# Kernel tuning notes

Measured on AMD Instinct MI355X. Metric: run time of the kernel, lower is better.

## Reference

```python
import jax, jax.numpy as jnp
import numpy as np

B, T, DIM = 4, 1024, 2048
N_HEADS, N_KV_HEADS = 32, 8
HEAD_DIM = DIM // N_HEADS  # 64
N_REPS = N_HEADS // N_KV_HEADS  # 4


def setup_inputs() -> dict:
    key = jax.random.key(0)
    ks = jax.random.split(key, 8)
    # RoPE tables: theta = 10000^{-2i/d}, positions 0..T-1
    inv_freq = 1.0 / (10000.0 ** (jnp.arange(0, HEAD_DIM, 2, dtype=jnp.float32) / HEAD_DIM))
    angles = jnp.arange(T, dtype=jnp.float32)[:, None] * inv_freq[None, :]  # (T, HEAD_DIM//2)
    s = 0.02
    return {
        "input": jax.random.normal(ks[0], (B, T, DIM), jnp.float32),
        "freqs_cos": jnp.cos(angles),
        "freqs_sin": jnp.sin(angles),
        "mask": jnp.tril(jnp.ones((T, T), dtype=bool)),  # causal boolean mask
        "wq": s * jax.random.normal(ks[1], (DIM, DIM), jnp.float32),
        "wk": s * jax.random.normal(ks[2], (N_KV_HEADS * HEAD_DIM, DIM), jnp.float32),
        "wv": s * jax.random.normal(ks[3], (N_KV_HEADS * HEAD_DIM, DIM), jnp.float32),
        "wo": s * jax.random.normal(ks[4], (DIM, DIM), jnp.float32),
        "curr_pos": 0,
    }


def _apply_rope(x, cos, sin):
    # x: (B, T, H, D); cos/sin: (T, D//2). Complex multiply on (even, odd) pairs.
    xr = x[..., 0::2]
    xi = x[..., 1::2]
    c = cos[None, :, None, :]
    s = sin[None, :, None, :]
    out_r = xr * c - xi * s
    out_i = xr * s + xi * c
    return jnp.stack([out_r, out_i], axis=-1).reshape(x.shape)


def reference(input, freqs_cos, freqs_sin, mask, wq, wk, wv, wo, curr_pos):
    Bv, Tv = input.shape[0], input.shape[1]
    qs = (input @ wq.T).reshape(Bv, Tv, N_HEADS, HEAD_DIM)
    ks = (input @ wk.T).reshape(Bv, Tv, N_KV_HEADS, HEAD_DIM)
    vs = (input @ wv.T).reshape(Bv, Tv, N_KV_HEADS, HEAD_DIM)
    qs = _apply_rope(qs, freqs_cos, freqs_sin)
    ks = _apply_rope(ks, freqs_cos, freqs_sin)

    # KV cache (prefill path: curr_pos == 0, fresh cache of length 2T)
    kv_cache = jnp.zeros((Bv, 2 * Tv, N_KV_HEADS, HEAD_DIM, 2), input.dtype)
    kv_cache = kv_cache.at[:, curr_pos:curr_pos + Tv, :, :, 0].set(ks)
    kv_cache = kv_cache.at[:, curr_pos:curr_pos + Tv, :, :, 1].set(vs)
    k_all = kv_cache[:, :curr_pos + Tv, :, :, 0]
    v_all = kv_cache[:, :curr_pos + Tv, :, :, 1]

    # GQA: broadcast each kv head across its query-head group (avoid repeat_interleave copy)
    S = k_all.shape[1]
    q = qs.transpose(0, 2, 1, 3).reshape(Bv, N_KV_HEADS, N_REPS, Tv, HEAD_DIM)
    k = k_all.transpose(0, 2, 1, 3)  # (B, KVH, S, D)
    v = v_all.transpose(0, 2, 1, 3)

    scale = 1.0 / jnp.sqrt(jnp.asarray(HEAD_DIM, input.dtype))
    scores = jnp.einsum("bgrqd,bgkd->bgrqk", q, k) * scale  # (B, KVH, REPS, T, S)
    neg = jnp.asarray(jnp.finfo(input.dtype).min, input.dtype)
    scores = jnp.where(mask[None, None, None, :, :S], scores, neg)
    attn = jax.nn.softmax(scores, axis=-1)
    out = jnp.einsum("bgrqk,bgkd->bgrqd", attn, v)
    out = out.reshape(Bv, N_HEADS, Tv, HEAD_DIM).transpose(0, 2, 1, 3).reshape(Bv, Tv, DIM)
    return out @ wo.T
```

## Files before the change

kernel.cpp:

```cpp
#include <hip/hip_runtime.h>
#include <cstdint>

typedef __bf16 bf16x8 __attribute__((ext_vector_type(8)));
typedef float  f32x4  __attribute__((ext_vector_type(4)));
typedef float  f32x16 __attribute__((ext_vector_type(16)));
typedef float  float8v __attribute__((ext_vector_type(8)));
typedef unsigned short ushort8v __attribute__((ext_vector_type(8)));
typedef unsigned short ushort4v __attribute__((ext_vector_type(4)));
typedef unsigned int   uint4v   __attribute__((ext_vector_type(4)));

__device__ __forceinline__ unsigned short f2b(float f) {
  uint32_t u = __builtin_bit_cast(uint32_t, f);
  u += 0x7FFFu + ((u >> 16) & 1u);
  return (unsigned short)(u >> 16);
}
__device__ __forceinline__ float b2f(unsigned short h) {
  uint32_t u = ((uint32_t)h) << 16;
  return __builtin_bit_cast(float, u);
}
__device__ __forceinline__ unsigned int cvtpk(float lo, float hi_) {
  unsigned int r;
  asm("v_cvt_pk_bf16_f32 %0, %1, %2" : "=v"(r) : "v"(lo), "v"(hi_));
  return r;
}

__device__ __forceinline__ void async16(const void* g, void* l) {
  __builtin_amdgcn_global_load_lds(
      (const __attribute__((address_space(1))) void*)g,
      (__attribute__((address_space(3))) void*)l, 16, 0, 0);
}

#define WAITVM(N)  __builtin_amdgcn_s_waitcnt(0x0F70 | ((N) & 15))
#define WAITLGKM0  __builtin_amdgcn_s_waitcnt(0xC07F)

struct CvtArgs {
  const float* src[5];
  unsigned short* dst[5];
  long n[5];
};
__global__ void cvt5_kernel(CvtArgs a) {
  long base = (long)blockIdx.x * blockDim.x + threadIdx.x;
  long gstride = (long)gridDim.x * blockDim.x;
#pragma unroll 1
  for (int sg = 0; sg < 5; ++sg) {
    const float* s = a.src[sg];
    unsigned short* d = a.dst[sg];
    long n8 = a.n[sg] >> 3;
    for (long i = base; i < n8; i += gstride) {
      float8v f = *(const float8v*)(s + i * 8);
      ushort8v o;
#pragma unroll
      for (int j = 0; j < 8; ++j) o[j] = f2b(f[j]);
      *(ushort8v*)(d + i * 8) = o;
    }
  }
}

template<bool F32OUT, int BN, int GX>
__global__ __launch_bounds__(512, 1)
void gemm8p(const unsigned short* __restrict__ Ag, const unsigned short* __restrict__ Wg,
            void* __restrict__ Cp, int M, int N) {
  constexpr int K = 2048;
  constexpr int NF = BN / 64;
  constexpr int BL = BN / 128;
  constexpr int VN = 4 + 2 * BL;
  constexpr int VT1 = (BN == 256) ? 6 : 4;
  constexpr int VT2 = (BN == 256) ? 4 : 3;
  constexpr int VT3 = (BN == 256) ? 2 : 1;
  constexpr int ASLOT = 16384;
  constexpr int BSLOT = BN * 64;
  constexpr int CPX = 2 * GX;

  extern __shared__ char lds_c[];

  const int tid = threadIdx.x;
  const int wave = tid >> 6, lane = tid & 63;
  const int wm = wave >> 2, wn = wave & 3;
  const int lr = lane & 15, lg = lane >> 4;

  const int flat = blockIdx.y * GX + blockIdx.x;
  const int swz = (flat & 7) * CPX + (flat >> 3);
  const int m0 = (swz / GX) * 256, n0 = (swz % GX) * BN;

  const int laneSw = (lr >> 1) * 128 + (((((lr & 1) << 2) | lg) ^ (lr >> 1)) << 4);
  const int aoff = wm * 8192 + laneSw;
  const int boff = wn * NF * 1024 + laneSw;

  f32x4 acc[8][NF] = {};

  auto stageHT = [&](int s) {
    const int ty = s & 3;
    const int kh = (s >> 1) & 1;
    const int buf = (s >> 2) & 1;
    const int kc = (s >> 2) * 64 + kh * 32;
    if (ty == 0 || ty == 2) {
      char* slot = lds_c + (buf * 2 + kh) * ASLOT;
#pragma unroll
      for (int j = 0; j < 2; ++j) {
        int q = (tid + 512 * j) * 16;
        int R = q >> 7, g2L = ((q >> 4) & 7) ^ (R & 7);
        int row = R * 2 + (g2L >> 2), kg = g2L & 3;
        async16(Ag + (size_t)(m0 + row) * K + kc + kg * 8, slot + q);
      }
    } else {
      char* slot = lds_c + 65536 + (buf * 2 + kh) * BSLOT;
#pragma unroll
      for (int j = 0; j < BL; ++j) {
        int q = (tid + 512 * j) * 16;
        int R = q >> 7, g2L = ((q >> 4) & 7) ^ (R & 7);
        int row = R * 2 + (g2L >> 2), kg = g2L & 3;
        async16(Wg + (size_t)(n0 + row) * K + kc + kg * 8, slot + q);
      }
    }
  };

#define PHASE(BUF, KH, MH, VM, ...)                                           \
  {                                                                           \
    const char* As_ = lds_c + ((BUF) * 2 + (KH)) * ASLOT;                     \
    const char* Bs_ = lds_c + 65536 + ((BUF) * 2 + (KH)) * BSLOT;             \
    bf16x8 af_[4], bf_[NF];                                                   \
    _Pragma("unroll") for (int mi = 0; mi < 4; ++mi)                          \
      af_[mi] = *(const bf16x8*)(As_ + aoff + (MH) * 4096 + mi * 1024);       \
    _Pragma("unroll") for (int ni = 0; ni < NF; ++ni)                         \
      bf_[ni] = *(const bf16x8*)(Bs_ + boff + ni * 1024);                     \
    __VA_ARGS__;                                                              \
    WAITVM(VM);                                                               \
    __builtin_amdgcn_s_barrier();                                             \
    WAITLGKM0;                                                                \
    __builtin_amdgcn_sched_barrier(0);                                        \
    __builtin_amdgcn_s_setprio(1);                                            \
    _Pragma("unroll") for (int mi = 0; mi < 4; ++mi)                          \
      _Pragma("unroll") for (int ni = 0; ni < NF; ++ni)                       \
        acc[(MH) * 4 + mi][ni] = __builtin_amdgcn_mfma_f32_16x16x32_bf16(     \
            af_[mi], bf_[ni], acc[(MH) * 4 + mi][ni], 0, 0, 0);               \
    __builtin_amdgcn_s_setprio(0);                                            \
    __builtin_amdgcn_s_barrier();                                             \
  }

#pragma unroll
  for (int s = 0; s < 6; ++s) stageHT(s);
  WAITVM(VN);
  __builtin_amdgcn_s_barrier();

#pragma unroll 2
  for (int kt = 0; kt < 30; ++kt) {
    const int buf = kt & 1;
    const int s0 = kt * 4 + 6;
    PHASE(buf, 0, 0, VN, stageHT(s0));
    PHASE(buf, 0, 1, VN, stageHT(s0 + 1));
    PHASE(buf, 1, 0, VN, stageHT(s0 + 2));
    PHASE(buf, 1, 1, VN, stageHT(s0 + 3));
  }
  PHASE(0, 0, 0, VN, stageHT(126));
  PHASE(0, 0, 1, VN, stageHT(127));
  PHASE(0, 1, 0, VT1, (void)0);
  PHASE(0, 1, 1, VT2, (void)0);
  PHASE(1, 0, 0, VT3, (void)0);
  PHASE(1, 0, 1, 0, (void)0);
  PHASE(1, 1, 0, 0, (void)0);
  PHASE(1, 1, 1, 0, (void)0);
#undef PHASE

#pragma unroll
  for (int mig = 0; mig < 8; ++mig) {
#pragma unroll
    for (int j = 0; j < 4; ++j) {
      int row = m0 + wm * 128 + mig * 16 + lg * 4 + j;
#pragma unroll
      for (int ni = 0; ni < NF; ++ni) {
        int col = n0 + wn * (NF * 16) + ni * 16 + lr;
        float v = acc[mig][ni][j];
        if (F32OUT) ((float*)Cp)[(size_t)row * N + col] = v;
        else        ((unsigned short*)Cp)[(size_t)row * N + col] = f2b(v);
      }
    }
  }
}

__global__ __launch_bounds__(256)
void ropekv_kernel(unsigned short* __restrict__ qkv,
                   const float* __restrict__ cosb, const float* __restrict__ sinb,
                   unsigned short* __restrict__ vt) {
  const int tt0 = blockIdx.x * 64;
  const int kvh = blockIdx.y;
  const int b   = blockIdx.z;
  const int tid = threadIdx.x;

  {
    int r = tid >> 2, c0 = (tid & 3) * 16;
    int t = tt0 + r;
    unsigned short* kp = qkv + (size_t)(b * 1024 + t) * 3072 + 2048 + kvh * 64 + c0;
    const float* cb = cosb + t * 32 + c0 / 2;
    const float* sb = sinb + t * 32 + c0 / 2;
    ushort8v x0 = *(const ushort8v*)kp;
    ushort8v x1 = *(const ushort8v*)(kp + 8);
    float8v c = *(const float8v*)cb;
    float8v s = *(const float8v*)sb;
    ushort8v o0, o1;
#pragma unroll
    for (int j = 0; j < 4; ++j) {
      float xr = b2f(x0[2 * j]), xi = b2f(x0[2 * j + 1]);
      o0[2 * j]     = f2b(xr * c[j] - xi * s[j]);
      o0[2 * j + 1] = f2b(xr * s[j] + xi * c[j]);
    }
#pragma unroll
    for (int j = 0; j < 4; ++j) {
      float xr = b2f(x1[2 * j]), xi = b2f(x1[2 * j + 1]);
      o1[2 * j]     = f2b(xr * c[4 + j] - xi * s[4 + j]);
      o1[2 * j + 1] = f2b(xr * s[4 + j] + xi * c[4 + j]);
    }
    *(ushort8v*)kp = o0;
    *(ushort8v*)(kp + 8) = o1;
  }

  __shared__ unsigned short lT[64 * 68];
#pragma unroll
  for (int i = 0; i < 2; ++i) {
    int r = i * 32 + (tid >> 3), c = (tid & 7) * 8;
    const unsigned short* src = qkv + (size_t)(b * 1024 + tt0 + r) * 3072 + 2560 + kvh * 64 + c;
    ushort8v v = *(const ushort8v*)src;
    ushort4v a, b4;
#pragma unroll
    for (int j = 0; j < 4; ++j) { a[j] = v[j]; b4[j] = v[j + 4]; }
    *(ushort4v*)&lT[r * 68 + c]     = a;
    *(ushort4v*)&lT[r * 68 + c + 4] = b4;
  }
  __syncthreads();
#pragma unroll
  for (int i = 0; i < 2; ++i) {
    int d = tid & 63;
    int tt = i * 4 + (tid >> 6);
    ushort8v o;
#pragma unroll
    for (int j = 0; j < 8; ++j) o[j] = lT[(tt * 8 + j) * 68 + d];
    *(ushort8v*)&vt[((size_t)((b * 8 + kvh) * 64 + d)) * 1024 + tt0 + tt * 8] = o;
  }
}

__global__ __launch_bounds__(256, 2)
void attn_kernel(const unsigned short* __restrict__ qkv, const unsigned short* __restrict__ vt,
                 const float* __restrict__ cosb, const float* __restrict__ sinb,
                 unsigned short* __restrict__ ob) {
  const int flat = (blockIdx.z * 8 + blockIdx.y) * 16 + blockIdx.x;
  const int swzb = (flat & 7) * 64 + (flat >> 3);
  const int bx = swzb & 15, kvh = (swzb >> 4) & 7, b = swzb >> 7;

  const int tid = threadIdx.x, wave = tid >> 6, lane = tid & 63;
  const int l31 = lane & 31, hi = lane >> 5;
  const int h = kvh * 4 + wave;

  const int qth = 31 - bx, qtl = bx;
  const int q0h = qth * 32, q0l = qtl * 32;
  const int nth = qth / 4 + 1, ntl = qtl / 4 + 1;
  const int ntot = nth + ntl;

  __shared__ unsigned short lK[2][128 * 64];
  __shared__ unsigned short lVt[2][64 * 128];

  auto ldq = [&](int q0, bf16x8* qf) {
    int t = q0 + l31;
    const unsigned short* qp = qkv + (size_t)(b * 1024 + t) * 3072 + h * 64;
#pragma unroll
    for (int dk = 0; dk < 4; ++dk) {
      ushort8v q = *(const ushort8v*)(qp + dk * 16 + hi * 8);
      f32x4 c4 = *(const f32x4*)(cosb + t * 32 + dk * 8 + hi * 4);
      f32x4 s4 = *(const f32x4*)(sinb + t * 32 + dk * 8 + hi * 4);
      ushort8v o;
#pragma unroll
      for (int j = 0; j < 4; ++j) {
        float xr = b2f(q[2 * j]), xi = b2f(q[2 * j + 1]);
        o[2 * j]     = f2b(xr * c4[j] - xi * s4[j]);
        o[2 * j + 1] = f2b(xr * s4[j] + xi * c4[j]);
      }
      qf[dk] = __builtin_bit_cast(bf16x8, o);
    }
  };

  const unsigned short* kg = qkv + (size_t)(b * 1024) * 3072 + 2048 + kvh * 64;
  const unsigned short* vg = vt + (size_t)(b * 8 + kvh) * 64 * 1024;

  auto stage = [&](int kvb, int bi) {
    const int sr  = tid >> 3;
    const int scb = (tid & 7) * 16;
#pragma unroll
    for (int i = 0; i < 4; ++i) {
      int r = i * 32 + sr;
      int cb = scb ^ ((r & 7) << 4);
      async16(kg + (size_t)(kvb + r) * 3072 + (cb >> 1), &lK[bi][r * 64 + (scb >> 1)]);
    }
    const int rv0 = tid >> 4;
    const int scv = (tid & 15) * 16;
#pragma unroll
    for (int i = 0; i < 4; ++i) {
      int rv = i * 16 + rv0;
      int cbv = scv ^ ((rv & 15) << 4);
      async16(vg + (size_t)rv * 1024 + kvb + (cbv >> 1), &lVt[bi][rv * 128 + (scv >> 1)]);
    }
  };

  bf16x8 qf[4];
  f32x16 oacc[2] = {};
  float m2 = -3e38f, l_run = 0.f;
  int q0 = q0h;

  ldq(q0h, qf);

  const float SC = 0.125f * 1.44269504f;

  auto chunk64 = [&](int cur, int ckvb, int c, bool lastT) {
    f32x16 sd[2] = {};
    __builtin_amdgcn_s_setprio(1);
#pragma unroll
    for (int s = 0; s < 2; ++s) {
      const int krow = c * 64 + s * 32 + l31;
      const char* kr = (const char*)lK[cur] + krow * 128;
      const int swz = (krow & 7) << 4;
#pragma unroll
      for (int dk = 0; dk < 4; ++dk) {
        bf16x8 kf = *(const bf16x8*)(kr + ((dk * 32 + hi * 16) ^ swz));
        sd[s] = __builtin_amdgcn_mfma_f32_32x32x16_bf16(kf, qf[dk], sd[s], 0, 0, 0);
      }
    }
    __builtin_amdgcn_s_setprio(0);

#pragma unroll
    for (int s = 0; s < 2; ++s)
#pragma unroll
      for (int r = 0; r < 16; ++r) {
        float v = sd[s][r] * SC;
        if (lastT) {
          int kvg = ckvb + s * 32 + (r & 3) + 8 * (r >> 2) + 4 * hi;
          if (kvg > q0 + l31) v = -3e38f;
        }
        sd[s][r] = v;
      }
    float pm = sd[0][0];
#pragma unroll
    for (int s = 0; s < 2; ++s)
#pragma unroll
      for (int r = 0; r < 16; ++r) pm = fmaxf(pm, sd[s][r]);
    pm = fmaxf(pm, __shfl_xor(pm, 32));
    if (!__all(pm <= m2 + 11.0f)) {
      float mnew = fmaxf(m2, pm);
      float alpha = exp2f(m2 - mnew);
      m2 = mnew;
      l_run *= alpha;
#pragma unroll
      for (int db = 0; db < 2; ++db)
#pragma unroll
        for (int r = 0; r < 16; ++r) oacc[db][r] *= alpha;
    }
    float tsum = 0.f;
#pragma unroll
    for (int s = 0; s < 2; ++s)
#pragma unroll
      for (int r = 0; r < 16; ++r) { float p = exp2f(sd[s][r] - m2); sd[s][r] = p; tsum += p; }
    tsum += __shfl_xor(tsum, 32);
    l_run += tsum;

    bf16x8 pf[2][2];
#pragma unroll
    for (int s = 0; s < 2; ++s)
#pragma unroll
      for (int kc = 0; kc < 2; ++kc) {
        unsigned int cA = cvtpk(sd[s][8 * kc + 0], sd[s][8 * kc + 1]);
        unsigned int cB = cvtpk(sd[s][8 * kc + 4], sd[s][8 * kc + 5]);
        unsigned int cC = cvtpk(sd[s][8 * kc + 2], sd[s][8 * kc + 3]);
        unsigned int cD = cvtpk(sd[s][8 * kc + 6], sd[s][8 * kc + 7]);
        unsigned int xA = __shfl_xor(cA, 32), xB = __shfl_xor(cB, 32);
        unsigned int xC = __shfl_xor(cC, 32), xD = __shfl_xor(cD, 32);
        uint4v u;
        u[0] = hi ? xB : cA;
        u[1] = hi ? xD : cC;
        u[2] = hi ? cB : xA;
        u[3] = hi ? cD : xC;
        pf[s][kc] = __builtin_bit_cast(bf16x8, u);
      }

    __builtin_amdgcn_s_setprio(1);
#pragma unroll
    for (int db = 0; db < 2; ++db) {
      const int row = db * 32 + l31;
      const char* vr = (const char*)lVt[cur] + row * 256;
      const int vswz = (row & 15) << 4;
#pragma unroll
      for (int s = 0; s < 2; ++s)
#pragma unroll
        for (int kc = 0; kc < 2; ++kc) {
          bf16x8 vf = *(const bf16x8*)(vr + ((c * 128 + s * 64 + kc * 32 + hi * 16) ^ vswz));
          oacc[db] = __builtin_amdgcn_mfma_f32_32x32x16_bf16(vf, pf[s][kc], oacc[db], 0, 0, 0);
        }
    }
    __builtin_amdgcn_s_setprio(0);
  };

  auto writeOut = [&](int q0w) {
    float inv = 1.0f / l_run;
    unsigned short* orow = ob + (size_t)(b * 1024 + q0w + l31) * 2048 + h * 64;
#pragma unroll
    for (int db = 0; db < 2; ++db)
#pragma unroll
      for (int g = 0; g < 4; ++g) {
        int d0 = db * 32 + 8 * g + 4 * hi;
        ushort4v o;
#pragma unroll
        for (int j = 0; j < 4; ++j) o[j] = f2b(oacc[db][4 * g + j] * inv);
        *(ushort4v*)(orow + d0) = o;
      }
  };

  auto kvb_of = [&](int j) { return (j < nth ? j : j - nth) * 128; };

  stage(0, 0);
  __syncthreads();

  for (int j = 0; j < ntot; ++j) {
    const int cur = j & 1;
    if (j + 1 < ntot) stage(kvb_of(j + 1), cur ^ 1);
    const int kvb = kvb_of(j);
    const bool lastT = (j == nth - 1) || (j == ntot - 1);

#pragma unroll 1
    for (int c = 0; c < 2; ++c) {
      if (kvb + c * 64 > q0 + 31) continue;
      chunk64(cur, kvb + c * 64, c, lastT);
    }

    if (j == nth - 1) {
      writeOut(q0h);
      oacc[0] = f32x16{}; oacc[1] = f32x16{};
      m2 = -3e38f; l_run = 0.f;
      q0 = q0l;
      ldq(q0l, qf);
    }
    __syncthreads();
  }
  writeOut(q0l);
}

extern "C" void kernel_launch(void* const* d_in, const int* in_sizes, int n_in,
                              void* d_out, int out_size, void* d_ws, size_t ws_size,
                              hipStream_t stream) {
  const float* input = (const float*)d_in[0];
  const float* fcos  = (const float*)d_in[1];
  const float* fsin  = (const float*)d_in[2];
  const float* wq = (const float*)d_in[4];
  const float* wk = (const float*)d_in[5];
  const float* wv = (const float*)d_in[6];
  const float* wo = (const float*)d_in[7];
  float* out = (float*)d_out;

  unsigned short* xb   = (unsigned short*)d_ws;
  unsigned short* wqkv = xb + (size_t)4096 * 2048;
  unsigned short* wob  = wqkv + (size_t)3072 * 2048;
  unsigned short* qkv  = wob + (size_t)2048 * 2048;
  unsigned short* ob   = qkv + (size_t)4096 * 3072;
  unsigned short* vtb  = xb;

  hipFuncSetAttribute((const void*)&gemm8p<false, 256, 12>,
                      hipFuncAttributeMaxDynamicSharedMemorySize, 131072);
  hipFuncSetAttribute((const void*)&gemm8p<true, 128, 16>,
                      hipFuncAttributeMaxDynamicSharedMemorySize, 98304);

  CvtArgs ca;
  ca.src[0] = input; ca.dst[0] = xb;                        ca.n[0] = (long)4096 * 2048;
  ca.src[1] = wq;    ca.dst[1] = wqkv;                      ca.n[1] = (long)2048 * 2048;
  ca.src[2] = wk;    ca.dst[2] = wqkv + (size_t)2048 * 2048; ca.n[2] = (long)512 * 2048;
  ca.src[3] = wv;    ca.dst[3] = wqkv + (size_t)2560 * 2048; ca.n[3] = (long)512 * 2048;
  ca.src[4] = wo;    ca.dst[4] = wob;                       ca.n[4] = (long)2048 * 2048;
  hipLaunchKernelGGL(cvt5_kernel, dim3(2048), dim3(256), 0, stream, ca);

  hipLaunchKernelGGL((gemm8p<false, 256, 12>), dim3(12, 16), dim3(512), 131072,
                     stream, xb, wqkv, (void*)qkv, 4096, 3072);

  hipLaunchKernelGGL(ropekv_kernel, dim3(16, 8, 4), dim3(256), 0, stream,
                     qkv, fcos, fsin, vtb);

  hipLaunchKernelGGL(attn_kernel, dim3(16, 8, 4), dim3(256), 0, stream,
                     qkv, vtb, fcos, fsin, ob);

  hipLaunchKernelGGL((gemm8p<true, 128, 16>), dim3(16, 16), dim3(512), 98304,
                     stream, ob, wob, (void*)out, 4096, 2048);
}
```

Baseline: 171.2 us.

## Rewrite GEMM pipeline as 4-slot ring with configurable BM and retiled output GEMM

```diff
diff --git a/kernel.cpp b/kernel.cpp
--- a/kernel.cpp
+++ b/kernel.cpp
@@ -56,20 +56,20 @@
   }
 }
 
-template<bool F32OUT, int BN, int GX>
-__global__ __launch_bounds__(512, 1)
-void gemm8p(const unsigned short* __restrict__ Ag, const unsigned short* __restrict__ Wg,
-            void* __restrict__ Cp, int M, int N) {
+template<bool F32OUT, int BM, int BN, int GX, int GY>
+__global__ __launch_bounds__(512, 2)
+void gemm2ph(const unsigned short* __restrict__ Ag, const unsigned short* __restrict__ Wg,
+             void* __restrict__ Cp, int N) {
   constexpr int K = 2048;
+  constexpr int MF = BM / 32;
   constexpr int NF = BN / 64;
+  constexpr int AL = BM / 128;
   constexpr int BL = BN / 128;
-  constexpr int VN = 4 + 2 * BL;
-  constexpr int VT1 = (BN == 256) ? 6 : 4;
-  constexpr int VT2 = (BN == 256) ? 4 : 3;
-  constexpr int VT3 = (BN == 256) ? 2 : 1;
-  constexpr int ASLOT = 16384;
+  constexpr int IPP = AL + BL;
+  constexpr int ASLOT = BM * 64;
   constexpr int BSLOT = BN * 64;
-  constexpr int CPX = 2 * GX;
+  constexpr int NWG = GX * GY;
+  constexpr int CPX = NWG / 8;
 
   extern __shared__ char lds_c[];
 
@@ -80,92 +80,83 @@
 
   const int flat = blockIdx.y * GX + blockIdx.x;
   const int swz = (flat & 7) * CPX + (flat >> 3);
-  const int m0 = (swz / GX) * 256, n0 = (swz % GX) * BN;
+  const int m0 = (swz / GX) * BM, n0 = (swz % GX) * BN;
 
   const int laneSw = (lr >> 1) * 128 + (((((lr & 1) << 2) | lg) ^ (lr >> 1)) << 4);
-  const int aoff = wm * 8192 + laneSw;
+  const int aoff = wm * (BM / 2) * 64 + laneSw;
   const int boff = wn * NF * 1024 + laneSw;
 
-  f32x4 acc[8][NF] = {};
-
-  auto stageHT = [&](int s) {
-    const int ty = s & 3;
-    const int kh = (s >> 1) & 1;
-    const int buf = (s >> 2) & 1;
-    const int kc = (s >> 2) * 64 + kh * 32;
-    if (ty == 0 || ty == 2) {
-      char* slot = lds_c + (buf * 2 + kh) * ASLOT;
-#pragma unroll
-      for (int j = 0; j < 2; ++j) {
-        int q = (tid + 512 * j) * 16;
-        int R = q >> 7, g2L = ((q >> 4) & 7) ^ (R & 7);
-        int row = R * 2 + (g2L >> 2), kg = g2L & 3;
-        async16(Ag + (size_t)(m0 + row) * K + kc + kg * 8, slot + q);
-      }
-    } else {
-      char* slot = lds_c + 65536 + (buf * 2 + kh) * BSLOT;
-#pragma unroll
-      for (int j = 0; j < BL; ++j) {
-        int q = (tid + 512 * j) * 16;
-        int R = q >> 7, g2L = ((q >> 4) & 7) ^ (R & 7);
-        int row = R * 2 + (g2L >> 2), kg = g2L & 3;
-        async16(Wg + (size_t)(n0 + row) * K + kc + kg * 8, slot + q);
-      }
-    }
-  };
-
-#define PHASE(BUF, KH, MH, VM, ...)                                           \
+  f32x4 acc[MF][NF] = {};
+
+  auto stageA = [&](int s) {
+    char* slot = lds_c + (s & 3) * ASLOT;
+    const int kc = s * 32;
+#pragma unroll
+    for (int j = 0; j < AL; ++j) {
+      int q = (tid + 512 * j) * 16;
+      int R = q >> 7, g2L = ((q >> 4) & 7) ^ (R & 7);
+      int row = R * 2 + (g2L >> 2), kg = g2L & 3;
+      async16(Ag + (size_t)(m0 + row) * K + kc + kg * 8, slot + q);
+    }
+  };
+  auto stageB = [&](int s) {
+    char* slot = lds_c + 4 * ASLOT + (s & 3) * BSLOT;
+    const int kc = s * 32;
+#pragma unroll
+    for (int j = 0; j < BL; ++j) {
+      int q = (tid + 512 * j) * 16;
+      int R = q >> 7, g2L = ((q >> 4) & 7) ^ (R & 7);
+      int row = R * 2 + (g2L >> 2), kg = g2L & 3;
+      async16(Wg + (size_t)(n0 + row) * K + kc + kg * 8, slot + q);
+    }
+  };
+
+#define PH(P, VM, DOST)                                                       \
   {                                                                           \
-    const char* As_ = lds_c + ((BUF) * 2 + (KH)) * ASLOT;                     \
-    const char* Bs_ = lds_c + 65536 + ((BUF) * 2 + (KH)) * BSLOT;             \
-    bf16x8 af_[4], bf_[NF];                                                   \
-    _Pragma("unroll") for (int mi = 0; mi < 4; ++mi)                          \
-      af_[mi] = *(const bf16x8*)(As_ + aoff + (MH) * 4096 + mi * 1024);       \
+    const char* As_ = lds_c + ((P) & 3) * ASLOT;                              \
+    const char* Bs_ = lds_c + 4 * ASLOT + ((P) & 3) * BSLOT;                  \
+    bf16x8 af_[MF], bf_[NF];                                                  \
+    _Pragma("unroll") for (int mi = 0; mi < MF; ++mi)                         \
+      af_[mi] = *(const bf16x8*)(As_ + aoff + mi * 1024);                     \
     _Pragma("unroll") for (int ni = 0; ni < NF; ++ni)                         \
       bf_[ni] = *(const bf16x8*)(Bs_ + boff + ni * 1024);                     \
-    __VA_ARGS__;                                                              \
+    if (DOST) { stageA((P) + 3); stageB((P) + 3); }                           \
     WAITVM(VM);                                                               \
     __builtin_amdgcn_s_barrier();                                             \
     WAITLGKM0;                                                                \
     __builtin_amdgcn_sched_barrier(0);                                        \
     __builtin_amdgcn_s_setprio(1);                                            \
-    _Pragma("unroll") for (int mi = 0; mi < 4; ++mi)                          \
+    _Pragma("unroll") for (int mi = 0; mi < MF; ++mi)                         \
       _Pragma("unroll") for (int ni = 0; ni < NF; ++ni)                       \
-        acc[(MH) * 4 + mi][ni] = __builtin_amdgcn_mfma_f32_16x16x32_bf16(     \
-            af_[mi], bf_[ni], acc[(MH) * 4 + mi][ni], 0, 0, 0);               \
+        acc[mi][ni] = __builtin_amdgcn_mfma_f32_16x16x32_bf16(                \
+            af_[mi], bf_[ni], acc[mi][ni], 0, 0, 0);                          \
     __builtin_amdgcn_s_setprio(0);                                            \
     __builtin_amdgcn_s_barrier();                                             \
   }
 
-#pragma unroll
-  for (int s = 0; s < 6; ++s) stageHT(s);
-  WAITVM(VN);
+  stageA(0); stageB(0);
+  stageA(1); stageB(1);
+  stageA(2); stageB(2);
+  WAITVM(2 * IPP);
   __builtin_amdgcn_s_barrier();
 
-#pragma unroll 2
-  for (int kt = 0; kt < 30; ++kt) {
-    const int buf = kt & 1;
-    const int s0 = kt * 4 + 6;
-    PHASE(buf, 0, 0, VN, stageHT(s0));
-    PHASE(buf, 0, 1, VN, stageHT(s0 + 1));
-    PHASE(buf, 1, 0, VN, stageHT(s0 + 2));
-    PHASE(buf, 1, 1, VN, stageHT(s0 + 3));
-  }
-  PHASE(0, 0, 0, VN, stageHT(126));
-  PHASE(0, 0, 1, VN, stageHT(127));
-  PHASE(0, 1, 0, VT1, (void)0);
-  PHASE(0, 1, 1, VT2, (void)0);
-  PHASE(1, 0, 0, VT3, (void)0);
-  PHASE(1, 0, 1, 0, (void)0);
-  PHASE(1, 1, 0, 0, (void)0);
-  PHASE(1, 1, 1, 0, (void)0);
-#undef PHASE
-
-#pragma unroll
-  for (int mig = 0; mig < 8; ++mig) {
+  for (int p2 = 0; p2 < 60; p2 += 4) {
+    PH(p2 + 0, 2 * IPP, true);
+    PH(p2 + 1, 2 * IPP, true);
+    PH(p2 + 2, 2 * IPP, true);
+    PH(p2 + 3, 2 * IPP, true);
+  }
+  PH(60, 2 * IPP, true);
+  PH(61, IPP, false);
+  PH(62, 0, false);
+  PH(63, 0, false);
+#undef PH
+
+#pragma unroll
+  for (int mig = 0; mig < MF; ++mig) {
 #pragma unroll
     for (int j = 0; j < 4; ++j) {
-      int row = m0 + wm * 128 + mig * 16 + lg * 4 + j;
+      int row = m0 + wm * (BM / 2) + mig * 16 + lg * 4 + j;
 #pragma unroll
       for (int ni = 0; ni < NF; ++ni) {
         int col = n0 + wn * (NF * 16) + ni * 16 + lr;
@@ -457,9 +448,9 @@
   unsigned short* ob   = qkv + (size_t)4096 * 3072;
   unsigned short* vtb  = xb;
 
-  hipFuncSetAttribute((const void*)&gemm8p<false, 256, 12>,
+  hipFuncSetAttribute((const void*)&gemm2ph<false, 256, 256, 12, 16>,
                       hipFuncAttributeMaxDynamicSharedMemorySize, 131072);
-  hipFuncSetAttribute((const void*)&gemm8p<true, 128, 16>,
+  hipFuncSetAttribute((const void*)&gemm2ph<true, 128, 256, 8, 32>,
                       hipFuncAttributeMaxDynamicSharedMemorySize, 98304);
 
   CvtArgs ca;
@@ -470,8 +461,8 @@
   ca.src[4] = wo;    ca.dst[4] = wob;                       ca.n[4] = (long)2048 * 2048;
   hipLaunchKernelGGL(cvt5_kernel, dim3(2048), dim3(256), 0, stream, ca);
 
-  hipLaunchKernelGGL((gemm8p<false, 256, 12>), dim3(12, 16), dim3(512), 131072,
-                     stream, xb, wqkv, (void*)qkv, 4096, 3072);
+  hipLaunchKernelGGL((gemm2ph<false, 256, 256, 12, 16>), dim3(12, 16), dim3(512), 131072,
+                     stream, xb, wqkv, (void*)qkv, 3072);
 
   hipLaunchKernelGGL(ropekv_kernel, dim3(16, 8, 4), dim3(256), 0, stream,
                      qkv, fcos, fsin, vtb);
@@ -479,6 +470,6 @@
   hipLaunchKernelGGL(attn_kernel, dim3(16, 8, 4), dim3(256), 0, stream,
                      qkv, vtb, fcos, fsin, ob);
 
-  hipLaunchKernelGGL((gemm8p<true, 128, 16>), dim3(16, 16), dim3(512), 98304,
-                     stream, ob, wob, (void*)out, 4096, 2048);
-}
+  hipLaunchKernelGGL((gemm2ph<true, 128, 256, 8, 32>), dim3(8, 32), dim3(512), 98304,
+                     stream, ob, wob, (void*)out, 2048);
+}
```

New measurement: 171.7 us. Within noise of the previous version (+0.3%).
